# Optimization experiments

Measured on AMD Instinct MI355X. Metric: run time of the kernel, lower is better.

## Reference

```python
import jax, jax.numpy as jnp
import numpy as np

B, L, D = 2, 1024, 768
N_LAYERS, D_STATE, D_CONV, EXPAND = 4, 16, 4, 2
D_INNER = EXPAND * D
DT_RANK = (D + 15) // 16  # 48, ceil(d_model/16) as in reference Mamba
N_CLS = 10
EPS = 1e-6


def rmsnorm(x, w):
    return x * jax.lax.rsqrt(jnp.mean(x * x, axis=-1, keepdims=True) + EPS) * w


def mamba_block(x, in_w, conv_w, conv_b, xp_w, dt_w, dt_b, A_log, D_skip, out_w):
    # x: (B, L, D)
    Bsz = x.shape[0]
    xz = jnp.einsum('bld,ed->ble', x, in_w)            # (B, L, 2*d_inner)
    xi, z = jnp.split(xz, 2, axis=-1)
    # causal depthwise conv over the sequence dim
    xc = jnp.transpose(xi, (0, 2, 1))                  # (B, d_inner, L)
    xc = jax.lax.conv_general_dilated(
        xc, conv_w[:, None, :], (1,), [(D_CONV - 1, 0)],
        dimension_numbers=('NCH', 'OIH', 'NCH'), feature_group_count=D_INNER)
    xc = jnp.transpose(xc, (0, 2, 1)) + conv_b         # (B, L, d_inner)
    xc = jax.nn.silu(xc)
    # input-dependent SSM parameters
    x_dbl = jnp.einsum('bld,ed->ble', xc, xp_w)        # (B, L, dt_rank + 2*d_state)
    dt, Bs, Cs = jnp.split(x_dbl, [DT_RANK, DT_RANK + D_STATE], axis=-1)
    delta = jax.nn.softplus(jnp.einsum('blr,dr->bld', dt, dt_w) + dt_b)  # (B, L, d_inner)
    A = -jnp.exp(A_log)                                # (d_inner, d_state)
    dA = jnp.exp(delta[..., None] * A)                 # (B, L, d_inner, d_state)
    dBu = delta[..., None] * Bs[:, :, None, :] * xc[..., None]

    def step(h, inp):
        dA_t, dBu_t, C_t = inp
        h = dA_t * h + dBu_t                           # (B, d_inner, d_state)
        y = jnp.einsum('bdn,bn->bd', h, C_t)
        return h, y

    h0 = jnp.zeros((Bsz, D_INNER, D_STATE), x.dtype)
    _, ys = jax.lax.scan(step, h0, (jnp.swapaxes(dA, 0, 1),
                                    jnp.swapaxes(dBu, 0, 1),
                                    jnp.swapaxes(Cs, 0, 1)))
    y = jnp.swapaxes(ys, 0, 1) + xc * D_skip           # (B, L, d_inner)
    y = y * jax.nn.silu(z)                             # gate
    return jnp.einsum('bld,od->blo', y, out_w)


def reference(x, norm_w, in_proj_w, conv_w, conv_b, x_proj_w, dt_proj_w, dt_proj_b,
              A_log, D_skip, out_proj_w, final_norm_w,
              head1_w, head1_b, head_norm_w, head2_w, head2_b):
    for i in range(N_LAYERS):
        res = x
        x = rmsnorm(x, norm_w[i])
        x = mamba_block(x, in_proj_w[i], conv_w[i], conv_b[i], x_proj_w[i],
                        dt_proj_w[i], dt_proj_b[i], A_log[i], D_skip[i],
                        out_proj_w[i]) + res
    x = rmsnorm(x, final_norm_w)
    last = x[:, -1, :]                                 # (B, D)
    h = last @ head1_w.T + head1_b
    h = rmsnorm(h, head_norm_w)
    h = jax.nn.gelu(h, approximate=False)              # torch nn.GELU default is exact erf
    return h @ head2_w.T + head2_b                     # (B, N_CLS)


def setup_inputs() -> dict:
    key = jax.random.key(0)
    ks = jax.random.split(key, 10)
    s = 0.02
    x = jax.random.normal(ks[0], (B, L, D), jnp.float32)
    norm_w = jnp.ones((N_LAYERS, D), jnp.float32)
    in_proj_w = s * jax.random.normal(ks[1], (N_LAYERS, 2 * D_INNER, D), jnp.float32)
    conv_w = s * jax.random.normal(ks[2], (N_LAYERS, D_INNER, D_CONV), jnp.float32)
    conv_b = jnp.zeros((N_LAYERS, D_INNER), jnp.float32)
    x_proj_w = s * jax.random.normal(ks[3], (N_LAYERS, DT_RANK + 2 * D_STATE, D_INNER), jnp.float32)
    dt_proj_w = s * jax.random.normal(ks[4], (N_LAYERS, D_INNER, DT_RANK), jnp.float32)
    dt_proj_b = jnp.full((N_LAYERS, D_INNER), -4.6, jnp.float32)  # softplus(-4.6) ~ 0.01
    A_log = jnp.log(jnp.broadcast_to(
        jnp.arange(1, D_STATE + 1, dtype=jnp.float32), (N_LAYERS, D_INNER, D_STATE)) + 0.0)
    D_skip = jnp.ones((N_LAYERS, D_INNER), jnp.float32)
    out_proj_w = s * jax.random.normal(ks[5], (N_LAYERS, D, D_INNER), jnp.float32)
    final_norm_w = jnp.ones((D,), jnp.float32)
    head1_w = s * jax.random.normal(ks[6], (D, D), jnp.float32)
    head1_b = jnp.zeros((D,), jnp.float32)
    head_norm_w = jnp.ones((D,), jnp.float32)
    head2_w = s * jax.random.normal(ks[7], (N_CLS, D), jnp.float32)
    head2_b = jnp.zeros((N_CLS,), jnp.float32)
    return {"x": x, "norm_w": norm_w, "in_proj_w": in_proj_w, "conv_w": conv_w,
            "conv_b": conv_b, "x_proj_w": x_proj_w, "dt_proj_w": dt_proj_w,
            "dt_proj_b": dt_proj_b, "A_log": A_log, "D_skip": D_skip,
            "out_proj_w": out_proj_w, "final_norm_w": final_norm_w,
            "head1_w": head1_w, "head1_b": head1_b, "head_norm_w": head_norm_w,
            "head2_w": head2_w, "head2_b": head2_b}
```

## Files before the change

### kernel.cpp

```cpp
#include <hip/hip_runtime.h>
#include <hip/hip_bf16.h>
#include <math.h>

typedef __bf16 bf16;
typedef __bf16 bf16x4 __attribute__((ext_vector_type(4)));
typedef __bf16 bf16x8 __attribute__((ext_vector_type(8)));
typedef float floatx4 __attribute__((ext_vector_type(4)));

#define BB 2
#define LL 1024
#define DD 768
#define DI 1536
#define MROWS 2048
#define NXP 80
#define DTRANK 48
#define DTPAD 64
#define DSTATE 16
#define NC 16
#define CLEN 64
#define KSPLIT 16
#define OPKS 4
#define LOG2E 1.4426950408889634f
#define TROW 132
#define SYROW 68

__device__ __forceinline__ void ld16(void* lds, const void* g) {
    __builtin_amdgcn_global_load_lds(
        (const __attribute__((address_space(1))) void*)g,
        (__attribute__((address_space(3))) void*)lds, 16, 0, 0);
}

__device__ __forceinline__ void wait_vm0() {
    asm volatile("s_waitcnt vmcnt(0)" ::: "memory");
}

__device__ __forceinline__ float row16_sum(float x) {
    float t;
    t = __int_as_float(__builtin_amdgcn_update_dpp(0, __float_as_int(x), 0x111, 0xF, 0xF, true)); x += t;
    t = __int_as_float(__builtin_amdgcn_update_dpp(0, __float_as_int(x), 0x112, 0xF, 0xF, true)); x += t;
    t = __int_as_float(__builtin_amdgcn_update_dpp(0, __float_as_int(x), 0x114, 0xF, 0xF, true)); x += t;
    t = __int_as_float(__builtin_amdgcn_update_dpp(0, __float_as_int(x), 0x118, 0xF, 0xF, true)); x += t;
    return x;
}

__device__ __forceinline__ float exp2_raw(float x) {
#if __has_builtin(__builtin_amdgcn_exp2f)
    return __builtin_amdgcn_exp2f(x);
#else
    float r; asm("v_exp_f32 %0, %1" : "=v"(r) : "v"(x)); return r;
#endif
}

#define N1 (4 * 3072 * 768)
#define N2 (4 * NXP * DI)
#define N3 (4 * DI * DTPAD)
#define N4 (4 * DD * DI)
__global__ __launch_bounds__(256) void cvt_all_k(const float* __restrict__ in_proj_w,
                                                 const float* __restrict__ x_proj_w,
                                                 const float* __restrict__ dt_proj_w,
                                                 const float* __restrict__ out_proj_w,
                                                 bf16* __restrict__ w_in,
                                                 bf16* __restrict__ w_xp,
                                                 bf16* __restrict__ w_dt,
                                                 bf16* __restrict__ w_out) {
    int i = blockIdx.x * 256 + threadIdx.x;
    if (i < N1) { w_in[i] = (bf16)in_proj_w[i]; return; }
    i -= N1;
    if (i < N2) { w_xp[i] = (bf16)x_proj_w[i]; return; }
    i -= N2;
    if (i < N3) {
        int row = i >> 6, c = i & 63;
        w_dt[i] = (c < DTRANK) ? (bf16)dt_proj_w[row * DTRANK + c] : (bf16)0.f;
        return;
    }
    i -= N3;
    if (i < N4) w_out[i] = (bf16)out_proj_w[i];
}

__global__ __launch_bounds__(256) void rmsnorm_k(const float* __restrict__ x,
                                                 const float* __restrict__ w,
                                                 bf16* __restrict__ out) {
    int row = blockIdx.x;
    const float* xr = x + (size_t)row * DD;
    int tid = threadIdx.x;
    float v[3]; float ss = 0.f;
    for (int j = 0; j < 3; j++) { v[j] = xr[tid + j * 256]; ss += v[j] * v[j]; }
    for (int o = 1; o < 64; o <<= 1) ss += __shfl_xor(ss, o, 64);
    __shared__ float sred[4];
    if ((tid & 63) == 0) sred[tid >> 6] = ss;
    __syncthreads();
    float scale = rsqrtf((sred[0] + sred[1] + sred[2] + sred[3]) / (float)DD + 1e-6f);
    for (int j = 0; j < 3; j++) {
        int c = tid + j * 256;
        out[(size_t)row * DD + c] = (bf16)(v[j] * scale * w[c]);
    }
}

template <int MODE>
__global__ __launch_bounds__(256) void gemm_bt(const bf16* __restrict__ A,
                                               const bf16* __restrict__ W,
                                               float* __restrict__ Cf,
                                               bf16* __restrict__ Cb,
                                               int M, int N, int K) {
    __shared__ bf16 As[128][32];
    __shared__ bf16 Ws[128][32];
    const int tid  = threadIdx.x;
    const int m0   = blockIdx.x * 128;
    const int n0   = blockIdx.y * 128;
    const int wave = tid >> 6;
    const int lane = tid & 63;
    const int wm   = (wave >> 1) * 64;
    const int wn   = (wave & 1) * 64;
    const int lrow = lane & 15;
    const int quad = lane >> 4;

    int kbeg = 0, kend = K;
    if constexpr (MODE == 5) {
        int kseg = K / gridDim.z;
        kbeg = blockIdx.z * kseg;
        kend = kbeg + kseg;
        Cf  += (size_t)blockIdx.z * M * N;
    }

    floatx4 acc[4][4];
    for (int mi = 0; mi < 4; mi++)
        for (int ni = 0; ni < 4; ni++) acc[mi][ni] = (floatx4){0.f, 0.f, 0.f, 0.f};

    const int r0  = tid >> 2;
    const int r1  = r0 + 64;
    const int seg = (tid & 3) * 8;
    char* asb0 = (char*)As + wave * 1024;
    char* asb1 = (char*)As + 4096 + wave * 1024;
    char* wsb0 = (char*)Ws + wave * 1024;
    char* wsb1 = (char*)Ws + 4096 + wave * 1024;

    for (int kb = kbeg; kb < kend; kb += 32) {
        int gk = kb + seg;
        __syncthreads();
        ld16(asb0, A + (size_t)(m0 + r0) * K + gk);
        ld16(asb1, A + (size_t)(m0 + r1) * K + gk);
        ld16(wsb0, W + (size_t)(n0 + r0) * K + gk);
        ld16(wsb1, W + (size_t)(n0 + r1) * K + gk);
        wait_vm0();
        __syncthreads();
        bf16x8 af[4], wf[4];
        for (int mi = 0; mi < 4; mi++) af[mi] = *(const bf16x8*)&As[wm + mi * 16 + lrow][quad * 8];
        for (int ni = 0; ni < 4; ni++) wf[ni] = *(const bf16x8*)&Ws[wn + ni * 16 + lrow][quad * 8];
        for (int mi = 0; mi < 4; mi++)
            for (int ni = 0; ni < 4; ni++)
                acc[mi][ni] = __builtin_amdgcn_mfma_f32_16x16x32_bf16(af[mi], wf[ni], acc[mi][ni], 0, 0, 0);
    }
    for (int mi = 0; mi < 4; mi++) {
        int rowb = m0 + wm + mi * 16 + quad * 4;
        for (int ni = 0; ni < 4; ni++) {
            int col = n0 + wn + ni * 16 + lrow;
            for (int r = 0; r < 4; r++) {
                int row = rowb + r;
                float v = acc[mi][ni][r];
                if constexpr (MODE == 1) Cb[(size_t)row * N + col] = (bf16)v;
                else                     Cf[(size_t)row * N + col] = v;
            }
        }
    }
}

__global__ __launch_bounds__(256) void op_reduce_norm_k(const float* __restrict__ part,
                                                        const float* __restrict__ resid,
                                                        const float* __restrict__ nw,
                                                        float* __restrict__ xout,
                                                        bf16* __restrict__ xnb) {
    int row = blockIdx.x;
    int tid = threadIdx.x;
    float v[3]; float ss = 0.f;
    for (int j = 0; j < 3; j++) {
        int c = tid + j * 256;
        size_t idx = (size_t)row * DD + c;
        float s = resid[idx];
        for (int ks = 0; ks < OPKS; ks++) s += part[(size_t)ks * MROWS * DD + idx];
        v[j] = s;
        xout[idx] = s;
        ss += s * s;
    }
    for (int o = 1; o < 64; o <<= 1) ss += __shfl_xor(ss, o, 64);
    __shared__ float sred[4];
    if ((tid & 63) == 0) sred[tid >> 6] = ss;
    __syncthreads();
    float scale = rsqrtf((sred[0] + sred[1] + sred[2] + sred[3]) / (float)DD + 1e-6f);
    for (int j = 0; j < 3; j++) {
        int c = tid + j * 256;
        xnb[(size_t)row * DD + c] = (bf16)(v[j] * scale * nw[c]);
    }
}

__global__ __launch_bounds__(256) void gemm_xp(const bf16* __restrict__ A,
                                               const bf16* __restrict__ W,
                                               float* __restrict__ part) {
    __shared__ bf16 As[64][40];
    __shared__ bf16 Ws[128][40];
    const int tid  = threadIdx.x;
    const int m0   = blockIdx.x * 64;
    const int ks   = blockIdx.y;
    const int k0   = ks * (DI / KSPLIT);
    const int wave = tid >> 6;
    const int lane = tid & 63;
    const int lrow = lane & 15;
    const int quad = lane >> 4;
    const int wm   = wave * 16;

    floatx4 acc[5];
    for (int ni = 0; ni < 5; ni++) acc[ni] = (floatx4){0.f, 0.f, 0.f, 0.f};

    const int ra  = tid >> 2;
    const int rw1 = ra + 64;
    const int seg = (tid & 3) * 8;

    for (int kb = 0; kb < DI / KSPLIT; kb += 32) {
        int gk = k0 + kb + seg;
        bf16x8 va = *(const bf16x8*)(A + (size_t)(m0 + ra) * DI + gk);
        bf16x8 vw0, vw1;
        if (ra < NXP) vw0 = *(const bf16x8*)(W + (size_t)ra * DI + gk);
        else          for (int j = 0; j < 8; j++) vw0[j] = (bf16)0.f;
        if (rw1 < NXP) vw1 = *(const bf16x8*)(W + (size_t)rw1 * DI + gk);
        else           for (int j = 0; j < 8; j++) vw1[j] = (bf16)0.f;
        __syncthreads();
        *(bf16x8*)&As[ra][seg]  = va;
        *(bf16x8*)&Ws[ra][seg]  = vw0;
        *(bf16x8*)&Ws[rw1][seg] = vw1;
        __syncthreads();
        bf16x8 af = *(const bf16x8*)&As[wm + lrow][quad * 8];
        for (int ni = 0; ni < 5; ni++) {
            bf16x8 wf = *(const bf16x8*)&Ws[ni * 16 + lrow][quad * 8];
            acc[ni] = __builtin_amdgcn_mfma_f32_16x16x32_bf16(af, wf, acc[ni], 0, 0, 0);
        }
    }
    float* pout = part + (size_t)ks * MROWS * NXP;
    for (int ni = 0; ni < 5; ni++) {
        int col = ni * 16 + lrow;
        for (int r = 0; r < 4; r++) {
            int row = m0 + wm + quad * 4 + r;
            pout[(size_t)row * NXP + col] = acc[ni][r];
        }
    }
}

__global__ __launch_bounds__(256) void xp_reduce_k(const float* __restrict__ part,
                                                   float* __restrict__ xdbl,
                                                   bf16* __restrict__ dtbf) {
    int idx = blockIdx.x * 256 + threadIdx.x;
    if (idx >= MROWS * NXP) return;
    float s = 0.f;
    for (int j = 0; j < KSPLIT; j++) s += part[(size_t)j * MROWS * NXP + idx];
    xdbl[idx] = s;
    int m = idx / NXP, c = idx - m * NXP;
    if (c < DTRANK)      dtbf[m * DTPAD + c] = (bf16)s;
    else if (c < DTPAD)  dtbf[m * DTPAD + c] = (bf16)0.f;
}

__global__ __launch_bounds__(256) void conv_silu_k(const bf16* __restrict__ xz,
                                                   const float* __restrict__ cw,
                                                   const float* __restrict__ cb,
                                                   bf16* __restrict__ xcb,
                                                   bf16* __restrict__ gzb) {
    int t = blockIdx.x * 256 + threadIdx.x;
    if (t >= MROWS * (DI / 4)) return;
    int m = t / (DI / 4);
    int d = (t - m * (DI / 4)) * 4;
    int l = m & (LL - 1);
    float acc[4];
    floatx4 cwv[4];
    for (int q = 0; q < 4; q++) {
        acc[q] = cb[d + q];
        cwv[q] = *(const floatx4*)&cw[(d + q) * 4];
    }
    for (int k = 0; k < 4; k++) {
        int lp = l - 3 + k;
        if (lp >= 0) {
            bf16x4 v = *(const bf16x4*)&xz[(size_t)(m - 3 + k) * (2 * DI) + d];
            for (int q = 0; q < 4; q++) acc[q] += (float)v[q] * cwv[q][k];
        }
    }
    bf16x4 xo, go;
    bf16x4 z4 = *(const bf16x4*)&xz[(size_t)m * (2 * DI) + DI + d];
    for (int q = 0; q < 4; q++) {
        float s = acc[q] / (1.f + __expf(-acc[q]));
        xo[q] = (bf16)s;
        float zv = (float)z4[q];
        go[q] = (bf16)(zv / (1.f + __expf(-zv)));
    }
    *(bf16x4*)&xcb[(size_t)m * DI + d] = xo;
    *(bf16x4*)&gzb[(size_t)m * DI + d] = go;
}

__global__ __launch_bounds__(256) void scan_k(const bf16* __restrict__ dtb,
                                              const bf16* __restrict__ wdt,
                                              const float* __restrict__ dtbias,
                                              const bf16* __restrict__ xcb,
                                              const bf16* __restrict__ gzb,
                                              const float* __restrict__ xdbl,
                                              const float* __restrict__ A_log,
                                              const float* __restrict__ Dskip,
                                              bf16* __restrict__ ybf) {
    const int b   = blockIdx.y;
    const int d0  = blockIdx.x * 16;
    const int tid = threadIdx.x;
    const int dl  = tid >> 4;
    const int n   = tid & 15;
    const int wv  = tid >> 6;
    const int lane = tid & 63;
    const int lr  = lane & 15;
    const int q   = lane >> 4;

    const float a2  = -__expf(A_log[(size_t)(d0 + dl) * DSTATE + n]) * LOG2E;
    const float bi  = dtbias[d0 + lr];
    const float dsk = Dskip[d0 + lr];

    __shared__ __align__(16) bf16  Bdt[16][72];
    __shared__ __align__(16) bf16  Adt[CLEN][64];
    __shared__ __align__(16) float sbcraw[CLEN][32];
    __shared__ __align__(16) bf16  sxc[CLEN][16];
    __shared__ __align__(16) bf16  sgz[CLEN][16];
    __shared__ __align__(16) float sdpT[16][TROW];
    __shared__ __align__(16) float sbcT[16][TROW];
    __shared__ float2 ssk[CLEN][16];
    __shared__ __align__(16) float syT[16][SYROW];

    auto stage = [&](int l0) {
        int s = tid, row = s >> 3, cc = s & 7;
        ld16((char*)&Adt[0][0] + (s & ~63) * 16,
             dtb + (size_t)(b * LL + l0 + row) * DTPAD + ((cc ^ (row & 7)) << 3));
        ld16((char*)&sbcraw[0][0] + (s & ~63) * 16,
             xdbl + (size_t)(b * LL + l0 + row) * NXP + DTRANK + cc * 4);
        s = tid + 256; row = s >> 3; cc = s & 7;
        ld16((char*)&Adt[0][0] + (s & ~63) * 16,
             dtb + (size_t)(b * LL + l0 + row) * DTPAD + ((cc ^ (row & 7)) << 3));
        ld16((char*)&sbcraw[0][0] + (s & ~63) * 16,
             xdbl + (size_t)(b * LL + l0 + row) * NXP + DTRANK + cc * 4);
        if (tid < 128) {
            int s2 = tid, r2 = s2 >> 1, c2 = s2 & 1;
            ld16((char*)&sxc[0][0] + (s2 & ~63) * 16,
                 xcb + (size_t)(b * LL + l0 + r2) * DI + d0 + c2 * 8);
        } else {
            int s2 = tid - 128, r2 = s2 >> 1, c2 = s2 & 1;
            ld16((char*)&sgz[0][0] + (s2 & ~63) * 16,
                 gzb + (size_t)(b * LL + l0 + r2) * DI + d0 + c2 * 8);
        }
    };

    stage(0);
    if (tid < 128) {
        int r = tid >> 3, s2 = (tid & 7) * 8;
        *(bf16x8*)&Bdt[r][s2] = *(const bf16x8*)&wdt[(size_t)(d0 + r) * DTPAD + s2];
    }
    wait_vm0();
    __syncthreads();

    float h = 0.f;
    for (int c = 0; c < NC; ++c) {
        const int l0 = c * CLEN;
        {
            floatx4 dacc = (floatx4){0.f, 0.f, 0.f, 0.f};
            const char* arow = (const char*)&Adt[16 * wv + lr][0];
            bf16x8 a0 = *(const bf16x8*)(arow + ((q ^ (lr & 7)) << 4));
            bf16x8 a1 = *(const bf16x8*)(arow + (((4 + q) ^ (lr & 7)) << 4));
            dacc = __builtin_amdgcn_mfma_f32_16x16x32_bf16(
                a0, *(const bf16x8*)&Bdt[lr][q * 8], dacc, 0, 0, 0);
            dacc = __builtin_amdgcn_mfma_f32_16x16x32_bf16(
                a1, *(const bf16x8*)&Bdt[lr][32 + q * 8], dacc, 0, 0, 0);
            #pragma unroll
            for (int r = 0; r < 4; ++r) {
                int l = 16 * wv + q * 4 + r;
                float v = dacc[r] + bi;
                v = (v > 20.f) ? v : log1pf(__expf(v));
                float xv = (float)sxc[l][lr];
                float gv = (float)sgz[l][lr];
                *(float2*)&sdpT[lr][2 * l] = make_float2(v, v * xv);
                ssk[l][lr] = make_float2(xv * dsk, gv);
            }
            #pragma unroll
            for (int k2 = 0; k2 < 4; ++k2) {
                int idx = tid + 256 * k2, ii = idx >> 4, dd = idx & 15;
                *(float2*)&sbcT[dd][2 * ii] =
                    make_float2(sbcraw[ii][dd], sbcraw[ii][16 + dd]);
            }
        }
        __syncthreads();
        if (c + 1 < NC) stage(l0 + CLEN);
        {
            const float4* dpr = (const float4*)&sdpT[dl][0];
            const float4* bcr = (const float4*)&sbcT[n][0];
            float4 dA[4], bA[4], dB[4], bB[4];
            float y4[4];
            #pragma unroll
            for (int t = 0; t < 4; ++t) { dA[t] = dpr[t]; bA[t] = bcr[t]; }
            #pragma unroll
            for (int g = 0; g < 8; ++g) {
                #pragma unroll
                for (int t = 0; t < 4; ++t) {
                    if (g + 1 < 8) {
                        if ((g & 1) == 0) { dB[t] = dpr[(g + 1) * 4 + t]; bB[t] = bcr[(g + 1) * 4 + t]; }
                        else              { dA[t] = dpr[(g + 1) * 4 + t]; bA[t] = bcr[(g + 1) * 4 + t]; }
                    }
                }
                #pragma unroll
                for (int t = 0; t < 8; ++t) {
                    float4 v = ((g & 1) == 0) ? dA[t >> 1] : dB[t >> 1];
                    float4 w = ((g & 1) == 0) ? bA[t >> 1] : bB[t >> 1];
                    float dvx = (t & 1) ? v.z : v.x;
                    float dpy = (t & 1) ? v.w : v.y;
                    float bx  = (t & 1) ? w.z : w.x;
                    float cy  = (t & 1) ? w.w : w.y;
                    float e = exp2_raw(dvx * a2);
                    h = __builtin_fmaf(e, h, dpy * bx);
                    y4[t & 3] = row16_sum(h * cy);
                    if ((t & 3) == 3 && n == 0) {
                        *(floatx4*)&syT[dl][g * 8 + t - 3] =
                            (floatx4){y4[0], y4[1], y4[2], y4[3]};
                    }
                }
            }
        }
        __syncthreads();
        wait_vm0();
        #pragma unroll
        for (int k2 = 0; k2 < 4; ++k2) {
            int idx = tid + 256 * k2, ii = idx >> 4, dd = idx & 15;
            float2 sk = ssk[ii][dd];
            float yv = (syT[dd][ii] + sk.x) * sk.y;
            ybf[(size_t)(b * LL + l0 + ii) * DI + d0 + dd] = (bf16)yv;
        }
        __syncthreads();
    }
}

__global__ __launch_bounds__(256) void head_norm_k(const float* __restrict__ x,
                                                   const float* __restrict__ fnw,
                                                   float* __restrict__ xn_buf) {
    int b = blockIdx.x;
    int tid = threadIdx.x;
    const float* xr = x + ((size_t)b * LL + (LL - 1)) * DD;
    __shared__ float sred[4];
    float v[3]; float ss = 0.f;
    for (int j = 0; j < 3; j++) { v[j] = xr[tid + j * 256]; ss += v[j] * v[j]; }
    for (int o = 1; o < 64; o <<= 1) ss += __shfl_xor(ss, o, 64);
    if ((tid & 63) == 0) sred[tid >> 6] = ss;
    __syncthreads();
    float scale = rsqrtf((sred[0] + sred[1] + sred[2] + sred[3]) / (float)DD + 1e-6f);
    for (int j = 0; j < 3; j++) {
        int c = tid + j * 256;
        xn_buf[(size_t)b * DD + c] = v[j] * scale * fnw[c];
    }
}

__global__ __launch_bounds__(256) void head_h1_k(const float* __restrict__ xn_buf,
                                                 const float* __restrict__ h1w,
                                                 const float* __restrict__ h1b,
                                                 float* __restrict__ h_buf) {
    int b  = blockIdx.x;
    int o0 = blockIdx.y * 64;
    int tid = threadIdx.x;
    __shared__ float sx[DD];
    for (int c = tid; c < DD; c += 256) sx[c] = xn_buf[(size_t)b * DD + c];
    __syncthreads();
    int wave = tid >> 6, lane = tid & 63;
    for (int j = 0; j < 16; j++) {
        int o = o0 + wave * 16 + j;
        const float* wrow = h1w + (size_t)o * DD;
        float acc = 0.f;
        for (int k = 0; k < 12; k++) {
            int c = lane + 64 * k;
            acc += wrow[c] * sx[c];
        }
        for (int off = 1; off < 64; off <<= 1) acc += __shfl_xor(acc, off, 64);
        if (lane == 0) h_buf[(size_t)b * DD + o] = acc + h1b[o];
    }
}

__global__ __launch_bounds__(256) void head_out_k(const float* __restrict__ h_buf,
                                                  const float* __restrict__ hnw,
                                                  const float* __restrict__ h2w,
                                                  const float* __restrict__ h2b,
                                                  float* __restrict__ out) {
    int b = blockIdx.x;
    int tid = threadIdx.x;
    __shared__ float hh[DD];
    __shared__ float sred[4];
    const float* hr = h_buf + (size_t)b * DD;
    float ss = 0.f;
    for (int c = tid; c < DD; c += 256) { float v = hr[c]; ss += v * v; }
    for (int o = 1; o < 64; o <<= 1) ss += __shfl_xor(ss, o, 64);
    if ((tid & 63) == 0) sred[tid >> 6] = ss;
    __syncthreads();
    float sc = rsqrtf((sred[0] + sred[1] + sred[2] + sred[3]) / (float)DD + 1e-6f);
    for (int c = tid; c < DD; c += 256) {
        float v = hr[c] * sc * hnw[c];
        hh[c] = 0.5f * v * (1.f + erff(v * 0.70710678118f));
    }
    __syncthreads();
    int w = tid >> 6, lane = tid & 63;
    for (int j = w; j < 10; j += 4) {
        float acc = 0.f;
        const float* wrow = h2w + (size_t)j * DD;
        for (int c = lane; c < DD; c += 64) acc += hh[c] * wrow[c];
        for (int o = 1; o < 64; o <<= 1) acc += __shfl_xor(acc, o, 64);
        if (lane == 0) out[b * 10 + j] = acc + h2b[j];
    }
}

extern "C" void kernel_launch(void* const* d_in, const int* in_sizes, int n_in,
                              void* d_out, int out_size, void* d_ws, size_t ws_size,
                              hipStream_t stream) {
    const float* x_in      = (const float*)d_in[0];
    const float* norm_w    = (const float*)d_in[1];
    const float* in_proj_w = (const float*)d_in[2];
    const float* conv_w    = (const float*)d_in[3];
    const float* conv_b    = (const float*)d_in[4];
    const float* x_proj_w  = (const float*)d_in[5];
    const float* dt_proj_w = (const float*)d_in[6];
    const float* dt_proj_b = (const float*)d_in[7];
    const float* A_log     = (const float*)d_in[8];
    const float* D_skip    = (const float*)d_in[9];
    const float* out_proj_w= (const float*)d_in[10];
    const float* fnw       = (const float*)d_in[11];
    const float* h1w       = (const float*)d_in[12];
    const float* h1b       = (const float*)d_in[13];
    const float* hnw       = (const float*)d_in[14];
    const float* h2w       = (const float*)d_in[15];
    const float* h2b       = (const float*)d_in[16];
    float* out = (float*)d_out;

    char* ws = (char*)d_ws;
    size_t off = 0;
    auto alloc = [&](size_t bytes) -> void* {
        void* p = ws + off;
        off += (bytes + 255) & ~(size_t)255;
        return p;
    };
    bf16* w_in  = (bf16*)alloc((size_t)N1 * 2);
    bf16* w_xp  = (bf16*)alloc((size_t)N2 * 2);
    bf16* w_dt  = (bf16*)alloc((size_t)N3 * 2);
    bf16* w_out = (bf16*)alloc((size_t)N4 * 2);
    bf16* xn_bf = (bf16*)alloc((size_t)MROWS * DD * 2);
    bf16* xz_bf = (bf16*)alloc((size_t)MROWS * 2 * DI * 2);
    bf16* xc_bf = (bf16*)alloc((size_t)MROWS * DI * 2);
    bf16* gz_bf = (bf16*)alloc((size_t)MROWS * DI * 2);
    float* xdbl = (float*)alloc((size_t)MROWS * NXP * 4);
    bf16* dt_bf = (bf16*)alloc((size_t)MROWS * DTPAD * 2);
    bf16* y_bf  = (bf16*)alloc((size_t)MROWS * DI * 2);
    float* x_buf= (float*)alloc((size_t)MROWS * DD * 4);
    float* xnl  = (float*)alloc((size_t)BB * DD * 4);
    float* hbuf = (float*)alloc((size_t)BB * DD * 4);
    float* xp_part = (float*)alloc((size_t)KSPLIT * MROWS * NXP * 4);
    float* op_part = (float*)alloc((size_t)OPKS * MROWS * DD * 4);

    {
        int ntot = N1 + N2 + N3 + N4;
        cvt_all_k<<<(ntot + 255) / 256, 256, 0, stream>>>(
            in_proj_w, x_proj_w, dt_proj_w, out_proj_w, w_in, w_xp, w_dt, w_out);
    }

    for (int i = 0; i < 4; i++) {
        const float* x_src = (i == 0) ? x_in : x_buf;
        if (i == 0)
            rmsnorm_k<<<MROWS, 256, 0, stream>>>(x_src, norm_w, xn_bf);
        gemm_bt<1><<<dim3(MROWS / 128, 3072 / 128), 256, 0, stream>>>(
            xn_bf, w_in + (size_t)i * 3072 * 768, nullptr, xz_bf,
            MROWS, 2 * DI, DD);
        conv_silu_k<<<(MROWS * (DI / 4) + 255) / 256, 256, 0, stream>>>(
            xz_bf, conv_w + (size_t)i * DI * 4, conv_b + (size_t)i * DI, xc_bf, gz_bf);
        gemm_xp<<<dim3(MROWS / 64, KSPLIT), 256, 0, stream>>>(
            xc_bf, w_xp + (size_t)i * NXP * DI, xp_part);
        xp_reduce_k<<<(MROWS * NXP + 255) / 256, 256, 0, stream>>>(xp_part, xdbl, dt_bf);
        scan_k<<<dim3(DI / 16, BB), 256, 0, stream>>>(
            dt_bf, w_dt + (size_t)i * DI * DTPAD, dt_proj_b + (size_t)i * DI,
            xc_bf, gz_bf, xdbl, A_log + (size_t)i * DI * DSTATE,
            D_skip + (size_t)i * DI, y_bf);
        gemm_bt<5><<<dim3(MROWS / 128, DD / 128, OPKS), 256, 0, stream>>>(
            y_bf, w_out + (size_t)i * DD * DI, op_part, nullptr,
            MROWS, DD, DI);
        op_reduce_norm_k<<<MROWS, 256, 0, stream>>>(
            op_part, x_src, norm_w + ((i + 1) & 3) * DD, x_buf, xn_bf);
    }

    head_norm_k<<<BB, 256, 0, stream>>>(x_buf, fnw, xnl);
    head_h1_k<<<dim3(BB, DD / 64), 256, 0, stream>>>(xnl, h1w, h1b, hbuf);
    head_out_k<<<BB, 256, 0, stream>>>(hbuf, hnw, h2w, h2b, out);
}
```

Baseline: 706.1 us.

## Split selective scan into chunked two-pass scan with carry composition

Replaces the sequential per-block scan over all 16 chunks with a chunk-parallel scheme. A first pass computes each chunk's local end state and decay product, a small compose kernel propagates carries across chunks, and a second pass rescans each chunk from its correct initial state to produce outputs. This spreads the work over NC times more blocks to fill the GPU, which the old 192-block grid could not. The cost is roughly doubled scan arithmetic, extra global traffic for the P/S/H0 buffers, and two extra kernel launches per layer.

```diff
diff --git a/kernel.cpp b/kernel.cpp
--- a/kernel.cpp
+++ b/kernel.cpp
@@ -291,17 +291,17 @@
     *(bf16x4*)&gzb[(size_t)m * DI + d] = go;
 }
 
-__global__ __launch_bounds__(256) void scan_k(const bf16* __restrict__ dtb,
-                                              const bf16* __restrict__ wdt,
-                                              const float* __restrict__ dtbias,
-                                              const bf16* __restrict__ xcb,
-                                              const bf16* __restrict__ gzb,
-                                              const float* __restrict__ xdbl,
-                                              const float* __restrict__ A_log,
-                                              const float* __restrict__ Dskip,
-                                              bf16* __restrict__ ybf) {
+__global__ __launch_bounds__(256) void scan1_k(const bf16* __restrict__ dtb,
+                                               const bf16* __restrict__ wdt,
+                                               const float* __restrict__ dtbias,
+                                               const bf16* __restrict__ xcb,
+                                               const float* __restrict__ xdbl,
+                                               const float* __restrict__ A_log,
+                                               float* __restrict__ Pbuf,
+                                               float* __restrict__ Sbuf) {
     const int b   = blockIdx.y;
     const int d0  = blockIdx.x * 16;
+    const int c   = blockIdx.z;
     const int tid = threadIdx.x;
     const int dl  = tid >> 4;
     const int n   = tid & 15;
@@ -309,22 +309,164 @@
     const int lane = tid & 63;
     const int lr  = lane & 15;
     const int q   = lane >> 4;
-
-    const float a2  = -__expf(A_log[(size_t)(d0 + dl) * DSTATE + n]) * LOG2E;
-    const float bi  = dtbias[d0 + lr];
-    const float dsk = Dskip[d0 + lr];
+    const int l0  = c * CLEN;
+
+    const float a2 = -__expf(A_log[(size_t)(d0 + dl) * DSTATE + n]) * LOG2E;
+    const float bi = dtbias[d0 + lr];
 
     __shared__ __align__(16) bf16  Bdt[16][72];
     __shared__ __align__(16) bf16  Adt[CLEN][64];
-    __shared__ __align__(16) float sbcraw[CLEN][32];
+    __shared__ __align__(16) float sbraw[CLEN][16];
+    __shared__ __align__(16) bf16  sxc[CLEN][16];
+    __shared__ __align__(16) float sdpT[16][TROW];
+    __shared__ __align__(16) float sbT[16][68];
+
+    {
+        int s = tid, row = s >> 3, cc = s & 7;
+        ld16((char*)&Adt[0][0] + (s & ~63) * 16,
+             dtb + (size_t)(b * LL + l0 + row) * DTPAD + ((cc ^ (row & 7)) << 3));
+        s = tid + 256; row = s >> 3; cc = s & 7;
+        ld16((char*)&Adt[0][0] + (s & ~63) * 16,
+             dtb + (size_t)(b * LL + l0 + row) * DTPAD + ((cc ^ (row & 7)) << 3));
+        {
+            int r2 = tid >> 2, c2 = tid & 3;
+            ld16((char*)&sbraw[0][0] + (tid & ~63) * 16,
+                 xdbl + (size_t)(b * LL + l0 + r2) * NXP + DTRANK + c2 * 4);
+        }
+        if (tid < 128) {
+            int r2 = tid >> 1, c2 = tid & 1;
+            ld16((char*)&sxc[0][0] + (tid & ~63) * 16,
+                 xcb + (size_t)(b * LL + l0 + r2) * DI + d0 + c2 * 8);
+            int r = tid >> 3, s2 = (tid & 7) * 8;
+            *(bf16x8*)&Bdt[r][s2] = *(const bf16x8*)&wdt[(size_t)(d0 + r) * DTPAD + s2];
+        }
+    }
+    wait_vm0();
+    __syncthreads();
+
+    {
+        floatx4 dacc = (floatx4){0.f, 0.f, 0.f, 0.f};
+        const char* arow = (const char*)&Adt[16 * wv + lr][0];
+        bf16x8 a0 = *(const bf16x8*)(arow + ((q ^ (lr & 7)) << 4));
+        bf16x8 a1 = *(const bf16x8*)(arow + (((4 + q) ^ (lr & 7)) << 4));
+        dacc = __builtin_amdgcn_mfma_f32_16x16x32_bf16(
+            a0, *(const bf16x8*)&Bdt[lr][q * 8], dacc, 0, 0, 0);
+        dacc = __builtin_amdgcn_mfma_f32_16x16x32_bf16(
+            a1, *(const bf16x8*)&Bdt[lr][32 + q * 8], dacc, 0, 0, 0);
+        float vv[4], xvv[4];
+        #pragma unroll
+        for (int r = 0; r < 4; ++r) {
+            int l = 16 * wv + q * 4 + r;
+            float v = dacc[r] + bi;
+            v = (v > 20.f) ? v : log1pf(__expf(v));
+            vv[r] = v; xvv[r] = (float)sxc[l][lr];
+        }
+        int L0 = 16 * wv + q * 4;
+        *(float4*)&sdpT[lr][2 * L0] =
+            make_float4(vv[0], vv[0] * xvv[0], vv[1], vv[1] * xvv[1]);
+        *(float4*)&sdpT[lr][2 * L0 + 4] =
+            make_float4(vv[2], vv[2] * xvv[2], vv[3], vv[3] * xvv[3]);
+        #pragma unroll
+        for (int k2 = 0; k2 < 4; ++k2) {
+            int idx = tid + 256 * k2, ii = idx >> 4, dd2 = idx & 15;
+            sbT[dd2][ii] = sbraw[ii][dd2];
+        }
+    }
+    __syncthreads();
+
+    float h = 0.f, sd = 0.f;
+    {
+        const float4* dpr = (const float4*)&sdpT[dl][0];
+        const float4* bpr = (const float4*)&sbT[n][0];
+        float4 dA[4], dB2[4], bA[2], bB2[2];
+        #pragma unroll
+        for (int t = 0; t < 4; ++t) dA[t] = dpr[t];
+        #pragma unroll
+        for (int t = 0; t < 2; ++t) bA[t] = bpr[t];
+        #pragma unroll
+        for (int g = 0; g < 8; ++g) {
+            if (g + 1 < 8) {
+                #pragma unroll
+                for (int t = 0; t < 4; ++t) {
+                    if ((g & 1) == 0) dB2[t] = dpr[(g + 1) * 4 + t];
+                    else              dA[t]  = dpr[(g + 1) * 4 + t];
+                }
+                #pragma unroll
+                for (int t = 0; t < 2; ++t) {
+                    if ((g & 1) == 0) bB2[t] = bpr[(g + 1) * 2 + t];
+                    else              bA[t]  = bpr[(g + 1) * 2 + t];
+                }
+            }
+            #pragma unroll
+            for (int i = 0; i < 8; ++i) {
+                float4 v = ((g & 1) == 0) ? dA[i >> 1] : dB2[i >> 1];
+                float4 w = ((g & 1) == 0) ? bA[i >> 2] : bB2[i >> 2];
+                float dvx = (i & 1) ? v.z : v.x;
+                float dpy = (i & 1) ? v.w : v.y;
+                float bx  = ((i & 3) == 0) ? w.x : ((i & 3) == 1) ? w.y
+                          : ((i & 3) == 2) ? w.z : w.w;
+                float e = exp2_raw(dvx * a2);
+                h = __builtin_fmaf(e, h, dpy * bx);
+                sd += dvx;
+            }
+        }
+    }
+    size_t o = (((size_t)c * BB + b) * DI + (d0 + dl)) * DSTATE + n;
+    Pbuf[o] = exp2_raw(a2 * sd);
+    Sbuf[o] = h;
+}
+
+__global__ __launch_bounds__(256) void compose_k(const float* __restrict__ P,
+                                                 const float* __restrict__ S,
+                                                 float* __restrict__ H0) {
+    int idx = blockIdx.x * 256 + threadIdx.x;
+    const size_t stride = (size_t)BB * DI * DSTATE;
+    float h = 0.f;
+    #pragma unroll
+    for (int c = 0; c < NC; ++c) {
+        H0[(size_t)c * stride + idx] = h;
+        h = __builtin_fmaf(P[(size_t)c * stride + idx], h, S[(size_t)c * stride + idx]);
+    }
+}
+
+__global__ __launch_bounds__(256) void scan2_k(const bf16* __restrict__ dtb,
+                                               const bf16* __restrict__ wdt,
+                                               const float* __restrict__ dtbias,
+                                               const bf16* __restrict__ xcb,
+                                               const bf16* __restrict__ gzb,
+                                               const float* __restrict__ xdbl,
+                                               const float* __restrict__ A_log,
+                                               const float* __restrict__ Dskip,
+                                               const float* __restrict__ H0buf,
+                                               bf16* __restrict__ ybf) {
+    const int b   = blockIdx.y;
+    const int d0  = blockIdx.x * 16;
+    const int c   = blockIdx.z;
+    const int tid = threadIdx.x;
+    const int dl  = tid >> 4;
+    const int n   = tid & 15;
+    const int wv  = tid >> 6;
+    const int lane = tid & 63;
+    const int lr  = lane & 15;
+    const int q   = lane >> 4;
+    const int l0  = c * CLEN;
+
+    const float a2 = -__expf(A_log[(size_t)(d0 + dl) * DSTATE + n]) * LOG2E;
+    const float bi = dtbias[d0 + lr];
+
+    __shared__ __align__(16) bf16  Bdt[16][72];
     __shared__ __align__(16) bf16  sxc[CLEN][16];
     __shared__ __align__(16) bf16  sgz[CLEN][16];
     __shared__ __align__(16) float sdpT[16][TROW];
     __shared__ __align__(16) float sbcT[16][TROW];
-    __shared__ float2 ssk[CLEN][16];
-    __shared__ __align__(16) float syT[16][SYROW];
-
-    auto stage = [&](int l0) {
+    __shared__ __align__(16) char  sov[16384];
+    bf16  (*Adt)[64]     = (bf16 (*)[64])sov;
+    float (*sbcraw)[32]  = (float (*)[32])(sov + 8192);
+    float (*syT)[SYROW]  = (float (*)[SYROW])sov;
+
+    float h = H0buf[((size_t)c * BB + b) * (DI * DSTATE) + (size_t)(d0 + dl) * DSTATE + n];
+
+    {
         int s = tid, row = s >> 3, cc = s & 7;
         ld16((char*)&Adt[0][0] + (s & ~63) * 16,
              dtb + (size_t)(b * LL + l0 + row) * DTPAD + ((cc ^ (row & 7)) << 3));
@@ -336,99 +478,94 @@
         ld16((char*)&sbcraw[0][0] + (s & ~63) * 16,
              xdbl + (size_t)(b * LL + l0 + row) * NXP + DTRANK + cc * 4);
         if (tid < 128) {
-            int s2 = tid, r2 = s2 >> 1, c2 = s2 & 1;
-            ld16((char*)&sxc[0][0] + (s2 & ~63) * 16,
+            int r2 = tid >> 1, c2 = tid & 1;
+            ld16((char*)&sxc[0][0] + (tid & ~63) * 16,
                  xcb + (size_t)(b * LL + l0 + r2) * DI + d0 + c2 * 8);
+            int r = tid >> 3, s2 = (tid & 7) * 8;
+            *(bf16x8*)&Bdt[r][s2] = *(const bf16x8*)&wdt[(size_t)(d0 + r) * DTPAD + s2];
         } else {
-            int s2 = tid - 128, r2 = s2 >> 1, c2 = s2 & 1;
-            ld16((char*)&sgz[0][0] + (s2 & ~63) * 16,
+            int t2 = tid - 128, r2 = t2 >> 1, c2 = t2 & 1;
+            ld16((char*)&sgz[0][0] + (t2 & ~63) * 16,
                  gzb + (size_t)(b * LL + l0 + r2) * DI + d0 + c2 * 8);
         }
-    };
-
-    stage(0);
-    if (tid < 128) {
-        int r = tid >> 3, s2 = (tid & 7) * 8;
-        *(bf16x8*)&Bdt[r][s2] = *(const bf16x8*)&wdt[(size_t)(d0 + r) * DTPAD + s2];
     }
     wait_vm0();
     __syncthreads();
 
-    float h = 0.f;
-    for (int c = 0; c < NC; ++c) {
-        const int l0 = c * CLEN;
-        {
-            floatx4 dacc = (floatx4){0.f, 0.f, 0.f, 0.f};
-            const char* arow = (const char*)&Adt[16 * wv + lr][0];
-            bf16x8 a0 = *(const bf16x8*)(arow + ((q ^ (lr & 7)) << 4));
-            bf16x8 a1 = *(const bf16x8*)(arow + (((4 + q) ^ (lr & 7)) << 4));
-            dacc = __builtin_amdgcn_mfma_f32_16x16x32_bf16(
-                a0, *(const bf16x8*)&Bdt[lr][q * 8], dacc, 0, 0, 0);
-            dacc = __builtin_amdgcn_mfma_f32_16x16x32_bf16(
-                a1, *(const bf16x8*)&Bdt[lr][32 + q * 8], dacc, 0, 0, 0);
+    {
+        floatx4 dacc = (floatx4){0.f, 0.f, 0.f, 0.f};
+        const char* arow = (const char*)&Adt[16 * wv + lr][0];
+        bf16x8 a0 = *(const bf16x8*)(arow + ((q ^ (lr & 7)) << 4));
+        bf16x8 a1 = *(const bf16x8*)(arow + (((4 + q) ^ (lr & 7)) << 4));
+        dacc = __builtin_amdgcn_mfma_f32_16x16x32_bf16(
+            a0, *(const bf16x8*)&Bdt[lr][q * 8], dacc, 0, 0, 0);
+        dacc = __builtin_amdgcn_mfma_f32_16x16x32_bf16(
+            a1, *(const bf16x8*)&Bdt[lr][32 + q * 8], dacc, 0, 0, 0);
+        float vv[4], xvv[4];
+        #pragma unroll
+        for (int r = 0; r < 4; ++r) {
+            int l = 16 * wv + q * 4 + r;
+            float v = dacc[r] + bi;
+            v = (v > 20.f) ? v : log1pf(__expf(v));
+            vv[r] = v; xvv[r] = (float)sxc[l][lr];
+        }
+        int L0 = 16 * wv + q * 4;
+        *(float4*)&sdpT[lr][2 * L0] =
+            make_float4(vv[0], vv[0] * xvv[0], vv[1], vv[1] * xvv[1]);
+        *(float4*)&sdpT[lr][2 * L0 + 4] =
+            make_float4(vv[2], vv[2] * xvv[2], vv[3], vv[3] * xvv[3]);
+        #pragma unroll
+        for (int k2 = 0; k2 < 4; ++k2) {
+            int idx = tid + 256 * k2, ii = idx >> 4, dd2 = idx & 15;
+            *(float2*)&sbcT[dd2][2 * ii] =
+                make_float2(sbcraw[ii][dd2], sbcraw[ii][16 + dd2]);
+        }
+    }
+    __syncthreads();
+
+    {
+        const float4* dpr = (const float4*)&sdpT[dl][0];
+        const float4* bcr = (const float4*)&sbcT[n][0];
+        float4 dA[4], bA[4], dB2[4], bB2[4];
+        float y4[4];
+        #pragma unroll
+        for (int t = 0; t < 4; ++t) { dA[t] = dpr[t]; bA[t] = bcr[t]; }
+        #pragma unroll
+        for (int g = 0; g < 8; ++g) {
             #pragma unroll
-            for (int r = 0; r < 4; ++r) {
-                int l = 16 * wv + q * 4 + r;
-                float v = dacc[r] + bi;
-                v = (v > 20.f) ? v : log1pf(__expf(v));
-                float xv = (float)sxc[l][lr];
-                float gv = (float)sgz[l][lr];
-                *(float2*)&sdpT[lr][2 * l] = make_float2(v, v * xv);
-                ssk[l][lr] = make_float2(xv * dsk, gv);
+            for (int t = 0; t < 4; ++t) {
+                if (g + 1 < 8) {
+                    if ((g & 1) == 0) { dB2[t] = dpr[(g + 1) * 4 + t]; bB2[t] = bcr[(g + 1) * 4 + t]; }
+                    else              { dA[t]  = dpr[(g + 1) * 4 + t]; bA[t]  = bcr[(g + 1) * 4 + t]; }
+                }
             }
             #pragma unroll
-            for (int k2 = 0; k2 < 4; ++k2) {
-                int idx = tid + 256 * k2, ii = idx >> 4, dd = idx & 15;
-                *(float2*)&sbcT[dd][2 * ii] =
-                    make_float2(sbcraw[ii][dd], sbcraw[ii][16 + dd]);
-            }
-        }
-        __syncthreads();
-        if (c + 1 < NC) stage(l0 + CLEN);
-        {
-            const float4* dpr = (const float4*)&sdpT[dl][0];
-            const float4* bcr = (const float4*)&sbcT[n][0];
-            float4 dA[4], bA[4], dB[4], bB[4];
-            float y4[4];
-            #pragma unroll
-            for (int t = 0; t < 4; ++t) { dA[t] = dpr[t]; bA[t] = bcr[t]; }
-            #pragma unroll
-            for (int g = 0; g < 8; ++g) {
-                #pragma unroll
-                for (int t = 0; t < 4; ++t) {
-                    if (g + 1 < 8) {
-                        if ((g & 1) == 0) { dB[t] = dpr[(g + 1) * 4 + t]; bB[t] = bcr[(g + 1) * 4 + t]; }
-                        else              { dA[t] = dpr[(g + 1) * 4 + t]; bA[t] = bcr[(g + 1) * 4 + t]; }
-                    }
-                }
-                #pragma unroll
-                for (int t = 0; t < 8; ++t) {
-                    float4 v = ((g & 1) == 0) ? dA[t >> 1] : dB[t >> 1];
-                    float4 w = ((g & 1) == 0) ? bA[t >> 1] : bB[t >> 1];
-                    float dvx = (t & 1) ? v.z : v.x;
-                    float dpy = (t & 1) ? v.w : v.y;
-                    float bx  = (t & 1) ? w.z : w.x;
-                    float cy  = (t & 1) ? w.w : w.y;
-                    float e = exp2_raw(dvx * a2);
-                    h = __builtin_fmaf(e, h, dpy * bx);
-                    y4[t & 3] = row16_sum(h * cy);
-                    if ((t & 3) == 3 && n == 0) {
-                        *(floatx4*)&syT[dl][g * 8 + t - 3] =
-                            (floatx4){y4[0], y4[1], y4[2], y4[3]};
-                    }
+            for (int i = 0; i < 8; ++i) {
+                float4 v = ((g & 1) == 0) ? dA[i >> 1] : dB2[i >> 1];
+                float4 w = ((g & 1) == 0) ? bA[i >> 1] : bB2[i >> 1];
+                float dvx = (i & 1) ? v.z : v.x;
+                float dpy = (i & 1) ? v.w : v.y;
+                float bx  = (i & 1) ? w.z : w.x;
+                float cy  = (i & 1) ? w.w : w.y;
+                float e = exp2_raw(dvx * a2);
+                h = __builtin_fmaf(e, h, dpy * bx);
+                y4[i & 3] = row16_sum(h * cy);
+                if ((i & 3) == 3 && n == 0) {
+                    *(floatx4*)&syT[dl][g * 8 + i - 3] =
+                        (floatx4){y4[0], y4[1], y4[2], y4[3]};
                 }
             }
         }
-        __syncthreads();
-        wait_vm0();
-        #pragma unroll
-        for (int k2 = 0; k2 < 4; ++k2) {
-            int idx = tid + 256 * k2, ii = idx >> 4, dd = idx & 15;
-            float2 sk = ssk[ii][dd];
-            float yv = (syT[dd][ii] + sk.x) * sk.y;
-            ybf[(size_t)(b * LL + l0 + ii) * DI + d0 + dd] = (bf16)yv;
-        }
-        __syncthreads();
+    }
+    __syncthreads();
+
+    #pragma unroll
+    for (int k2 = 0; k2 < 4; ++k2) {
+        int idx = tid + 256 * k2, ii = idx >> 4, dd = idx & 15;
+        float xv = (float)sxc[ii][dd];
+        float gv = (float)sgz[ii][dd];
+        float yv = (syT[dd][ii] + xv * Dskip[d0 + dd]) * gv;
+        ybf[(size_t)(b * LL + l0 + ii) * DI + d0 + dd] = (bf16)yv;
     }
 }
 
@@ -547,6 +684,9 @@
     bf16* dt_bf = (bf16*)alloc((size_t)MROWS * DTPAD * 2);
     bf16* y_bf  = (bf16*)alloc((size_t)MROWS * DI * 2);
     float* x_buf= (float*)alloc((size_t)MROWS * DD * 4);
+    float* Pbuf = (float*)alloc((size_t)NC * BB * DI * DSTATE * 4);
+    float* Sbuf = (float*)alloc((size_t)NC * BB * DI * DSTATE * 4);
+    float* H0buf= (float*)alloc((size_t)NC * BB * DI * DSTATE * 4);
     float* xnl  = (float*)alloc((size_t)BB * DD * 4);
     float* hbuf = (float*)alloc((size_t)BB * DD * 4);
     float* xp_part = (float*)alloc((size_t)KSPLIT * MROWS * NXP * 4);
@@ -570,10 +710,14 @@
         gemm_xp<<<dim3(MROWS / 64, KSPLIT), 256, 0, stream>>>(
             xc_bf, w_xp + (size_t)i * NXP * DI, xp_part);
         xp_reduce_k<<<(MROWS * NXP + 255) / 256, 256, 0, stream>>>(xp_part, xdbl, dt_bf);
-        scan_k<<<dim3(DI / 16, BB), 256, 0, stream>>>(
+        scan1_k<<<dim3(DI / 16, BB, NC), 256, 0, stream>>>(
+            dt_bf, w_dt + (size_t)i * DI * DTPAD, dt_proj_b + (size_t)i * DI,
+            xc_bf, xdbl, A_log + (size_t)i * DI * DSTATE, Pbuf, Sbuf);
+        compose_k<<<(BB * DI * DSTATE) / 256, 256, 0, stream>>>(Pbuf, Sbuf, H0buf);
+        scan2_k<<<dim3(DI / 16, BB, NC), 256, 0, stream>>>(
             dt_bf, w_dt + (size_t)i * DI * DTPAD, dt_proj_b + (size_t)i * DI,
             xc_bf, gz_bf, xdbl, A_log + (size_t)i * DI * DSTATE,
-            D_skip + (size_t)i * DI, y_bf);
+            D_skip + (size_t)i * DI, H0buf, y_bf);
         gemm_bt<5><<<dim3(MROWS / 128, DD / 128, OPKS), 256, 0, stream>>>(
             y_bf, w_out + (size_t)i * DD * DI, op_part, nullptr,
             MROWS, DD, DI);
```

After: 658.5 us. 6.7% less time.
